# Performance work log

Measured on AMD Instinct MI355X. Metric: run time of the kernel, lower is better.

Reference implementation:

```python
import jax, jax.numpy as jnp
import numpy as np

IN_F = 1024
OUT_F = 1024
GRID_SIZE = 5
SPLINE_ORDER = 3
GRID_RANGE = (-1.0, 1.0)


def _make_grid():
    h = (GRID_RANGE[1] - GRID_RANGE[0]) / GRID_SIZE
    g = jnp.arange(-SPLINE_ORDER, GRID_SIZE + SPLINE_ORDER + 1, dtype=jnp.float32) * h + GRID_RANGE[0]
    return jnp.broadcast_to(g, (IN_F, g.shape[0]))  # (F, grid_size + 2*order + 1)


def setup_inputs() -> dict:
    key = jax.random.key(0)
    k1, k2, k3, k4 = jax.random.split(key, 4)
    B = 8192
    x = jax.random.normal(k1, (B, IN_F), dtype=jnp.float32)
    base_weight = jax.random.normal(k2, (OUT_F, IN_F), dtype=jnp.float32) / np.sqrt(IN_F)
    # mimic reset_parameters: uniform noise scaled by scale_noise/grid_size
    spline_weight = (jax.random.uniform(k3, (OUT_F, IN_F, GRID_SIZE + SPLINE_ORDER)) - 0.5) * (0.1 / GRID_SIZE)
    spline_scaler = jax.random.normal(k4, (OUT_F, IN_F), dtype=jnp.float32) / np.sqrt(IN_F)
    grid = _make_grid()
    return {"x": x, "base_weight": base_weight, "spline_weight": spline_weight,
            "spline_scaler": spline_scaler, "grid": grid}


def b_splines(x, grid):
    # x: (B, F); grid: (F, G) with G = grid_size + 2*order + 1
    xe = x[:, :, None]  # (B, F, 1)
    bases = ((xe >= grid[:, :-1]) & (xe < grid[:, 1:])).astype(x.dtype)  # (B, F, G-1)
    for k in range(1, SPLINE_ORDER + 1):
        left = (xe - grid[:, : -(k + 1)]) / (grid[:, k:-1] - grid[:, : -(k + 1)])
        right = (grid[:, k + 1 :] - xe) / (grid[:, k + 1 :] - grid[:, 1:-k])
        bases = left * bases[:, :, :-1] + right * bases[:, :, 1:]
    return bases  # (B, F, grid_size + order)


def reference(x, base_weight, spline_weight, spline_scaler, grid):
    base_out = jax.nn.silu(x) @ base_weight.T  # (B, O)
    basis = b_splines(x, grid)  # (B, F, C)
    scaled_w = spline_weight * spline_scaler[:, :, None]  # (O, F, C)
    spline_out = jnp.einsum('bfc,ofc->bo', basis, scaled_w)
    return base_out + spline_out
```

## Files before the change

kernel.cpp:

```cpp
#include <hip/hip_runtime.h>
#include <hip/hip_bf16.h>

#define IN_F   1024
#define OUT_F  1024
#define NCH    9
#define KDIM   9216
#define BATCH  8192
#define NELEM  (BATCH * OUT_F)

#define BM 256
#define BN 256
#define BK 32
#define KHALF 4608
#define NTK (KHALF / BK)
#define SLOT 16384

typedef __attribute__((ext_vector_type(4)))  float  f32x4;
typedef __attribute__((ext_vector_type(8)))  __bf16 bf16x8;

typedef __attribute__((address_space(3))) unsigned short       lds_u16;
typedef const __attribute__((address_space(1))) unsigned short glb_u16;

__device__ inline unsigned short f2bf(float f) {
    union { float f; unsigned int u; } v; v.f = f;
    unsigned int u = v.u;
    unsigned int r = (u + 0x7FFFu + ((u >> 16) & 1u)) >> 16;
    return (unsigned short)r;
}

__global__ void prep_kernel(const float* __restrict__ x,
                            const float* __restrict__ bw,
                            const float* __restrict__ sw,
                            const float* __restrict__ sc,
                            unsigned short* __restrict__ A,
                            unsigned short* __restrict__ W) {
    const int bid = blockIdx.x;
    if (bid < 4096) {
        int idx = bid * 256 + threadIdx.x;
        const float4* xp = (const float4*)(x + (size_t)idx * 8);
        float4 x0 = xp[0], x1 = xp[1];
        float xs[8] = {x0.x, x0.y, x0.z, x0.w, x1.x, x1.y, x1.z, x1.w};

        unsigned short vals[8][9];
#pragma unroll
        for (int e = 0; e < 8; ++e) {
            float v  = xs[e];
            float s  = v / (1.0f + __expf(-v));
            float t  = (v + 2.2f) * 2.5f;
            float jf = floorf(t);
            int   j  = (int)jf;
            float u  = t - jf;
            float u2 = u * u, u3 = u2 * u;
            float p0 = u3 * (1.0f / 6.0f);
            float p1 = (-3.0f * u3 + 3.0f * u2 + 3.0f * u + 1.0f) * (1.0f / 6.0f);
            float p2 = (3.0f * u3 - 6.0f * u2 + 4.0f) * (1.0f / 6.0f);
            float om = 1.0f - u;
            float p3 = om * om * om * (1.0f / 6.0f);
            bool valid = (v >= -2.2f) && (v < 2.2f);
#pragma unroll
            for (int c = 0; c < 8; ++c) {
                int p = j - c;
                float bv = 0.0f;
                if (valid)
                    bv = (p == 0) ? p0 : (p == 1) ? p1 : (p == 2) ? p2 : (p == 3) ? p3 : 0.0f;
                vals[e][c] = f2bf(bv);
            }
            vals[e][8] = f2bf(s);
        }

        int r = idx >> 7, f8 = idx & 127;
        unsigned short* base = A + (size_t)r * KDIM + f8 * 8;
#pragma unroll
        for (int c = 0; c < 9; ++c) {
            uint4 pk;
            pk.x = (unsigned int)vals[0][c] | ((unsigned int)vals[1][c] << 16);
            pk.y = (unsigned int)vals[2][c] | ((unsigned int)vals[3][c] << 16);
            pk.z = (unsigned int)vals[4][c] | ((unsigned int)vals[5][c] << 16);
            pk.w = (unsigned int)vals[6][c] | ((unsigned int)vals[7][c] << 16);
            *(uint4*)(base + (size_t)c * 1024) = pk;
        }
    } else {
        int idx = (bid - 4096) * 256 + threadIdx.x;
        int o = idx >> 10, f = idx & 1023;
        float scale = sc[idx];
        const float4* swp = (const float4*)(sw + (size_t)idx * 8);
        float4 w0 = swp[0], w1 = swp[1];
        unsigned short* Wb = W + (size_t)o * KDIM + f;
        Wb[0 * 1024] = f2bf(w0.x * scale);
        Wb[1 * 1024] = f2bf(w0.y * scale);
        Wb[2 * 1024] = f2bf(w0.z * scale);
        Wb[3 * 1024] = f2bf(w0.w * scale);
        Wb[4 * 1024] = f2bf(w1.x * scale);
        Wb[5 * 1024] = f2bf(w1.y * scale);
        Wb[6 * 1024] = f2bf(w1.z * scale);
        Wb[7 * 1024] = f2bf(w1.w * scale);
        Wb[8 * 1024] = f2bf(bw[idx]);
    }
}

#define DECLS(q) \
    const int ci##q = (q) * 512 + tid; \
    const int lo##q = ci##q << 3; \
    const int rr##q = ci##q >> 2; \
    const int cl##q = (((ci##q & 3) ^ ((rr##q >> 1) & 3)) << 3); \
    const unsigned short* srcA##q = Ap + (size_t)(m0 + rr##q) * KDIM + kbase + cl##q; \
    const unsigned short* srcB##q = Wp + (size_t)(n0 + rr##q) * KDIM + kbase + cl##q;

#define STAGE_A(q, ns) do { \
    __builtin_amdgcn_global_load_lds((glb_u16*)srcA##q, (lds_u16*)(ns) + lo##q, 16, 0, 0); \
    srcA##q += BK; } while (0)

#define STAGE_B(q, ns) do { \
    __builtin_amdgcn_global_load_lds((glb_u16*)srcB##q, (lds_u16*)(ns) + 8192 + lo##q, 16, 0, 0); \
    srcB##q += BK; } while (0)

#define RDA(mi) (*(const bf16x8*)&sA[(rowa + (mi) * 16) * BK + koff])
#define RDB(ni) (*(const bf16x8*)&sB[(rowb + (ni) * 16) * BK + koff])

#define MM4(av, mi) \
    acc[mi][0] = __builtin_amdgcn_mfma_f32_16x16x32_bf16(av, b0, acc[mi][0], 0, 0, 0); \
    acc[mi][1] = __builtin_amdgcn_mfma_f32_16x16x32_bf16(av, b1, acc[mi][1], 0, 0, 0); \
    acc[mi][2] = __builtin_amdgcn_mfma_f32_16x16x32_bf16(av, b2, acc[mi][2], 0, 0, 0); \
    acc[mi][3] = __builtin_amdgcn_mfma_f32_16x16x32_bf16(av, b3, acc[mi][3], 0, 0, 0);

__global__ __launch_bounds__(512, 2) void gemm_ring(
    const unsigned short* __restrict__ Ap,
    const unsigned short* __restrict__ Wp,
    float* __restrict__ C, float* __restrict__ P, int mode) {
    __shared__ unsigned short lds[4 * SLOT];

    const int tid  = threadIdx.x;
    const int wave = tid >> 6;
    const int lane = tid & 63;
    const int lm16 = lane & 15;
    const int lhi  = lane >> 4;
    const int koff = ((lhi ^ ((lm16 >> 1) & 3)) << 3);

    const int bid  = blockIdx.x;
    const int mg   = bid & 3;
    const int kb   = (bid >> 2) & 1;
    const int j    = bid >> 3;
    const int m0   = (mg * 8 + (j >> 2)) * BM;
    const int n0   = (j & 3) * BN;
    const int kbase = kb * KHALF;

    const int wr = wave >> 2;
    const int wc = wave & 3;
    const int rowa = wr * 128 + lm16;
    const int rowb = wc * 64 + lm16;

    f32x4 acc[8][4];
#pragma unroll
    for (int i = 0; i < 8; ++i)
#pragma unroll
        for (int jn = 0; jn < 4; ++jn) acc[i][jn] = (f32x4)(0.0f);

    DECLS(0) DECLS(1)

    {
        unsigned short* ns = lds;
        STAGE_A(0, ns); STAGE_A(1, ns); STAGE_B(0, ns); STAGE_B(1, ns);
    }
    {
        unsigned short* ns = lds + SLOT;
        STAGE_A(0, ns); STAGE_A(1, ns); STAGE_B(0, ns); STAGE_B(1, ns);
    }
    {
        unsigned short* ns = lds + 2 * SLOT;
        STAGE_A(0, ns); STAGE_A(1, ns); STAGE_B(0, ns); STAGE_B(1, ns);
    }
    asm volatile("s_waitcnt vmcnt(8)" ::: "memory");
    __builtin_amdgcn_s_barrier();

#pragma unroll 4
    for (int t = 0; t < NTK; ++t) {
        const unsigned short* sA = lds + (t & 3) * SLOT;
        const unsigned short* sB = sA + 8192;
        unsigned short* ns = lds + ((t + 3) & 3) * SLOT;

        if (t + 3 < NTK) { STAGE_A(0, ns); STAGE_A(1, ns); STAGE_B(0, ns); STAGE_B(1, ns); }

        bf16x8 b0 = RDB(0), b1 = RDB(1), b2 = RDB(2), b3 = RDB(3);
        __builtin_amdgcn_s_setprio(1);
        bf16x8 a0 = RDA(0); MM4(a0, 0)
        bf16x8 a1 = RDA(1); MM4(a1, 1)
        bf16x8 a2 = RDA(2); MM4(a2, 2)
        bf16x8 a3 = RDA(3); MM4(a3, 3)
        bf16x8 a4 = RDA(4); MM4(a4, 4)
        bf16x8 a5 = RDA(5); MM4(a5, 5)
        bf16x8 a6 = RDA(6); MM4(a6, 6)
        bf16x8 a7 = RDA(7); MM4(a7, 7)
        __builtin_amdgcn_s_setprio(0);

        if (t <= NTK - 4)      asm volatile("s_waitcnt vmcnt(8)" ::: "memory");
        else if (t == NTK - 3) asm volatile("s_waitcnt vmcnt(4)" ::: "memory");
        else                   asm volatile("s_waitcnt vmcnt(0)" ::: "memory");
        __builtin_amdgcn_s_barrier();
    }

    const int orow = m0 + wr * 128 + (lhi << 2);
    const int ocol = n0 + wc * 64 + lm16;
    if (mode) {
#pragma unroll
        for (int mi = 0; mi < 8; ++mi)
#pragma unroll
            for (int ni = 0; ni < 4; ++ni)
#pragma unroll
                for (int r = 0; r < 4; ++r)
                    atomicAdd(&C[(size_t)(orow + mi * 16 + r) * OUT_F + (ocol + ni * 16)], acc[mi][ni][r]);
    } else {
        float* dst = kb ? P : C;
#pragma unroll
        for (int mi = 0; mi < 8; ++mi)
#pragma unroll
            for (int ni = 0; ni < 4; ++ni)
#pragma unroll
                for (int r = 0; r < 4; ++r)
                    dst[(size_t)(orow + mi * 16 + r) * OUT_F + (ocol + ni * 16)] = acc[mi][ni][r];
    }
}

__global__ void add_kernel(float* __restrict__ C, const float* __restrict__ P) {
    int i = blockIdx.x * blockDim.x + threadIdx.x;
    if (i >= NELEM / 4) return;
    f32x4* c4 = (f32x4*)C;
    const f32x4* p4 = (const f32x4*)P;
    c4[i] = c4[i] + p4[i];
}

extern "C" void kernel_launch(void* const* d_in, const int* in_sizes, int n_in,
                              void* d_out, int out_size, void* d_ws, size_t ws_size,
                              hipStream_t stream) {
    const float* x             = (const float*)d_in[0];
    const float* base_weight   = (const float*)d_in[1];
    const float* spline_weight = (const float*)d_in[2];
    const float* spline_scaler = (const float*)d_in[3];
    float* out = (float*)d_out;

    const size_t wbytes = (size_t)OUT_F * KDIM * 2;
    const size_t abytes = (size_t)BATCH * KDIM * 2;
    const size_t pbytes = (size_t)NELEM * 4;
    unsigned short* Wc   = (unsigned short*)d_ws;
    unsigned short* Abuf = (unsigned short*)((char*)d_ws + wbytes);
    float*          P    = (float*)((char*)d_ws + wbytes + abytes);

    const int mode = (ws_size >= wbytes + abytes + pbytes) ? 0 : 1;
    if (mode == 1)
        (void)hipMemsetAsync(d_out, 0, pbytes, stream);

    prep_kernel<<<8192, 256, 0, stream>>>(x, base_weight, spline_weight,
                                          spline_scaler, Abuf, Wc);

    gemm_ring<<<256, 512, 0, stream>>>(Abuf, Wc, out, P, mode);

    if (mode == 0)
        add_kernel<<<(NELEM / 4 + 255) / 256, 256, 0, stream>>>(out, P);
}
```

Before: 199.1 us.

## Restructure GEMM ring into double-pair buffering with half the barriers

The 4-slot ring pipeline, which staged one K-tile per iteration with a partial vmcnt wait and a barrier each step, becomes a two-pair ping-pong: each iteration computes two K-tiles from one pair of LDS slots while loading the next two tiles into the other pair, then does a full vmcnt(0) wait and a single barrier. This halves the number of barriers and simplifies the wait logic. In exchange, prefetch depth shrinks (up to two tiles ahead instead of three) and each iteration waits for all outstanding loads, which may expose more global-memory latency. NTK=144 is a multiple of 4, so the loop covers every tile.

```diff
diff --git a/kernel.cpp b/kernel.cpp
--- a/kernel.cpp
+++ b/kernel.cpp
@@ -123,7 +123,38 @@
     acc[mi][2] = __builtin_amdgcn_mfma_f32_16x16x32_bf16(av, b2, acc[mi][2], 0, 0, 0); \
     acc[mi][3] = __builtin_amdgcn_mfma_f32_16x16x32_bf16(av, b3, acc[mi][3], 0, 0, 0);
 
-__global__ __launch_bounds__(512, 2) void gemm_ring(
+#define TILE_BODY(sbase) do { \
+    const unsigned short* sA = lds + (sbase); \
+    const unsigned short* sB = sA + 8192; \
+    bf16x8 b0 = RDB(0), b1 = RDB(1), b2 = RDB(2), b3 = RDB(3); \
+    __builtin_amdgcn_s_setprio(1); \
+    bf16x8 a0 = RDA(0); MM4(a0, 0) \
+    bf16x8 a1 = RDA(1); MM4(a1, 1) \
+    bf16x8 a2 = RDA(2); MM4(a2, 2) \
+    bf16x8 a3 = RDA(3); MM4(a3, 3) \
+    bf16x8 a4 = RDA(4); MM4(a4, 4) \
+    bf16x8 a5 = RDA(5); MM4(a5, 5) \
+    bf16x8 a6 = RDA(6); MM4(a6, 6) \
+    bf16x8 a7 = RDA(7); MM4(a7, 7) \
+    __builtin_amdgcn_s_setprio(0); \
+} while (0)
+
+#define ITER(T, cs) do { \
+    if ((T) + 2 < NTK) { \
+        unsigned short* ns0 = lds + (((cs) ^ 2)) * SLOT; \
+        STAGE_A(0, ns0); STAGE_A(1, ns0); STAGE_B(0, ns0); STAGE_B(1, ns0); \
+    } \
+    if ((T) + 3 < NTK) { \
+        unsigned short* ns1 = lds + (((cs) ^ 2) + 1) * SLOT; \
+        STAGE_A(0, ns1); STAGE_A(1, ns1); STAGE_B(0, ns1); STAGE_B(1, ns1); \
+    } \
+    TILE_BODY((cs) * SLOT); \
+    TILE_BODY(((cs) + 1) * SLOT); \
+    asm volatile("s_waitcnt vmcnt(0)" ::: "memory"); \
+    __builtin_amdgcn_s_barrier(); \
+} while (0)
+
+__global__ __launch_bounds__(512, 2) void gemm_ring2(
     const unsigned short* __restrict__ Ap,
     const unsigned short* __restrict__ Wp,
     float* __restrict__ C, float* __restrict__ P, int mode) {
@@ -165,37 +196,13 @@
         unsigned short* ns = lds + SLOT;
         STAGE_A(0, ns); STAGE_A(1, ns); STAGE_B(0, ns); STAGE_B(1, ns);
     }
-    {
-        unsigned short* ns = lds + 2 * SLOT;
-        STAGE_A(0, ns); STAGE_A(1, ns); STAGE_B(0, ns); STAGE_B(1, ns);
-    }
-    asm volatile("s_waitcnt vmcnt(8)" ::: "memory");
+    asm volatile("s_waitcnt vmcnt(0)" ::: "memory");
     __builtin_amdgcn_s_barrier();
 
-#pragma unroll 4
-    for (int t = 0; t < NTK; ++t) {
-        const unsigned short* sA = lds + (t & 3) * SLOT;
-        const unsigned short* sB = sA + 8192;
-        unsigned short* ns = lds + ((t + 3) & 3) * SLOT;
-
-        if (t + 3 < NTK) { STAGE_A(0, ns); STAGE_A(1, ns); STAGE_B(0, ns); STAGE_B(1, ns); }
-
-        bf16x8 b0 = RDB(0), b1 = RDB(1), b2 = RDB(2), b3 = RDB(3);
-        __builtin_amdgcn_s_setprio(1);
-        bf16x8 a0 = RDA(0); MM4(a0, 0)
-        bf16x8 a1 = RDA(1); MM4(a1, 1)
-        bf16x8 a2 = RDA(2); MM4(a2, 2)
-        bf16x8 a3 = RDA(3); MM4(a3, 3)
-        bf16x8 a4 = RDA(4); MM4(a4, 4)
-        bf16x8 a5 = RDA(5); MM4(a5, 5)
-        bf16x8 a6 = RDA(6); MM4(a6, 6)
-        bf16x8 a7 = RDA(7); MM4(a7, 7)
-        __builtin_amdgcn_s_setprio(0);
-
-        if (t <= NTK - 4)      asm volatile("s_waitcnt vmcnt(8)" ::: "memory");
-        else if (t == NTK - 3) asm volatile("s_waitcnt vmcnt(4)" ::: "memory");
-        else                   asm volatile("s_waitcnt vmcnt(0)" ::: "memory");
-        __builtin_amdgcn_s_barrier();
+#pragma unroll 1
+    for (int t2 = 0; t2 < NTK; t2 += 4) {
+        ITER(t2, 0);
+        ITER(t2 + 2, 2);
     }
 
     const int orow = m0 + wr * 128 + (lhi << 2);
@@ -251,7 +258,7 @@
     prep_kernel<<<8192, 256, 0, stream>>>(x, base_weight, spline_weight,
                                           spline_scaler, Abuf, Wc);
 
-    gemm_ring<<<256, 512, 0, stream>>>(Abuf, Wc, out, P, mode);
+    gemm_ring2<<<256, 512, 0, stream>>>(Abuf, Wc, out, P, mode);
 
     if (mode == 0)
         add_kernel<<<(NELEM / 4 + 255) / 256, 256, 0, stream>>>(out, P);
```

Measured after the change: 225.1 us. 1.13x slower.
